# Kernel optimization log

Hardware: AMD Instinct MI355X
Metric: run time of the kernel (lower is better)

## Reference

```python
import jax, jax.numpy as jnp
import numpy as np

B, S, D, V = 2, 2048, 1024, 32000
EPSILON = 5.0


def setup_inputs() -> dict:
    key = jax.random.key(0)
    k1, k2, k3, k4 = jax.random.split(key, 4)
    inputs_embeds = jax.random.normal(k1, (B, S, D), dtype=jnp.float32)
    table = jax.random.normal(k2, (V, D), dtype=jnp.float32)
    # dx-privacy noise: unit-norm Gaussian direction * Gamma(alpha=D, rate=eps*D) scalar sample
    noise_v = jax.random.normal(k3, (B, S, D), dtype=jnp.float32)
    norm = jnp.linalg.norm(noise_v, axis=-1, keepdims=True)
    norm = jnp.where(norm > 0, norm, jnp.ones_like(norm))
    gamma_scale = jax.random.gamma(k4, jnp.float32(D)) / jnp.float32(EPSILON * D)
    noise = gamma_scale * (noise_v / norm)
    return {"inputs_embeds": inputs_embeds, "table": table, "noise": noise}


def reference(inputs_embeds, table, noise):
    # perturb embeddings with precomputed dx-privacy noise (no_grad in original)
    perturbed = inputs_embeds + noise                      # [B,S,D]
    # full similarity matrix vs vocabulary, then nearest-embedding snap
    sims = jnp.einsum('bsd,vd->bsv', perturbed, table)     # [B,S,V]
    max_token = jnp.argmax(sims, axis=-1)                  # [B,S] int
    res = jnp.take(table, max_token, axis=0)               # [B,S,D]
    return res
```

## Files before the change

kernel.cpp:

```cpp
#include <hip/hip_runtime.h>
#include <stdint.h>

#define ROWS 4096
#define DIM 1024
#define VOCAB 32000
#define BM 128
#define BN 128
#define NTILES (VOCAB / BN)
#define NCHUNKS 24
#define SCALE 2048.0f

typedef float floatx4 __attribute__((ext_vector_type(4)));
typedef _Float16 f16x8 __attribute__((ext_vector_type(8)));
typedef _Float16 f16x4 __attribute__((ext_vector_type(4)));

__device__ __forceinline__ void load_lds16(const _Float16* g, _Float16* l) {
    __builtin_amdgcn_global_load_lds(
        (const __attribute__((address_space(1))) uint32_t*)g,
        (__attribute__((address_space(3))) uint32_t*)l, 16, 0, 0);
}

__global__ void init_keys(unsigned long long* __restrict__ keys) {
    int i = blockIdx.x * 256 + threadIdx.x;
    if (i < ROWS) keys[i] = 0ull;
}

__global__ void split_sum(const float* __restrict__ x, const float* __restrict__ y,
                          _Float16* __restrict__ hi, _Float16* __restrict__ lo) {
    size_t i = ((size_t)blockIdx.x * 256 + threadIdx.x) * 8;
    floatx4 a = *(const floatx4*)(x + i);
    floatx4 b = *(const floatx4*)(x + i + 4);
    floatx4 c = *(const floatx4*)(y + i);
    floatx4 d = *(const floatx4*)(y + i + 4);
    f16x8 h, l;
#pragma unroll
    for (int j = 0; j < 4; j++) {
        float p = (a[j] + c[j]) * SCALE;
        _Float16 hh = (_Float16)p;
        h[j] = hh; l[j] = (_Float16)(p - (float)hh);
        float q = (b[j] + d[j]) * SCALE;
        _Float16 hq = (_Float16)q;
        h[4 + j] = hq; l[4 + j] = (_Float16)(q - (float)hq);
    }
    *(f16x8*)(hi + i) = h;
    *(f16x8*)(lo + i) = l;
}

__global__ void split_one(const float* __restrict__ x,
                          _Float16* __restrict__ hi, _Float16* __restrict__ lo) {
    size_t i = ((size_t)blockIdx.x * 256 + threadIdx.x) * 8;
    floatx4 a = *(const floatx4*)(x + i);
    floatx4 b = *(const floatx4*)(x + i + 4);
    f16x8 h, l;
#pragma unroll
    for (int j = 0; j < 4; j++) {
        float p = a[j] * SCALE;
        _Float16 hh = (_Float16)p;
        h[j] = hh; l[j] = (_Float16)(p - (float)hh);
        float q = b[j] * SCALE;
        _Float16 hq = (_Float16)q;
        h[4 + j] = hq; l[4 + j] = (_Float16)(q - (float)hq);
    }
    *(f16x8*)(hi + i) = h;
    *(f16x8*)(lo + i) = l;
}

__global__ __launch_bounds__(256, 3) void gemm_argmax_pre(
    const _Float16* __restrict__ Ah, const _Float16* __restrict__ Al,
    const _Float16* __restrict__ Bh, const _Float16* __restrict__ Bl,
    unsigned long long* __restrict__ keys) {
    __shared__ __align__(16) _Float16 sAh[BM * 32];
    __shared__ __align__(16) _Float16 sAl[BM * 32];
    __shared__ __align__(16) _Float16 sBh[BN * 32];
    __shared__ __align__(16) _Float16 sBl[BN * 32];
    __shared__ unsigned long long redk[BM];

    const int tid = threadIdx.x;
    const int w = tid >> 6, lane = tid & 63;
    const int quad = lane >> 4, lq = lane & 15;
    const int rb = blockIdx.x / NCHUNKS, chunk = blockIdx.x % NCHUNKS;
    const int row0 = rb * BM;
    const int wm = (w & 1) * 64, wn = (w >> 1) * 64;
    const int tstart = chunk * NTILES / NCHUNKS;
    const int tend = (chunk + 1) * NTILES / NCHUNKS;

    if (tid < BM) redk[tid] = 0ull;

    union PF { f16x8 v; _Float16 s[8]; } fidx, fone;
#pragma unroll
    for (int j = 0; j < 8; j++) { fidx.s[j] = (_Float16)0.0f; fone.s[j] = (_Float16)0.0f; }
    if (quad == 0) { fidx.s[0] = (_Float16)(float)lq; fone.s[0] = (_Float16)1.0f; }
    floatx4 c1 = {0.f, 0.f, 0.f, 0.f}, c2 = {0.f, 0.f, 0.f, 0.f};
    c1 = __builtin_amdgcn_mfma_f32_16x16x32_f16(fidx.v, fone.v, c1, 0, 0, 0);
    c2 = __builtin_amdgcn_mfma_f32_16x16x32_f16(fone.v, fidx.v, c2, 0, 0, 0);
    int m_of[4], n_of[4];
#pragma unroll
    for (int r = 0; r < 4; r++) {
        m_of[r] = (int)(c1[r] + 0.5f);
        n_of[r] = (int)(c2[r] + 0.5f);
    }

    const _Float16* gsrcA = (w == 0) ? (Ah + (size_t)row0 * DIM)
                        : (w == 1) ? (Al + (size_t)row0 * DIM)
                        : (w == 2) ? Bh : Bl;
    _Float16* ldst = (w == 0) ? sAh : (w == 1) ? sAl : (w == 2) ? sBh : sBl;

    float rmax[16];
    int ridx[16];
#pragma unroll
    for (int i = 0; i < 16; i++) { rmax[i] = -3.4e38f; ridx[i] = 0; }

    for (int t = tstart; t < tend; ++t) {
        const int n0 = t * BN;
        const _Float16* gsrc = (w < 2) ? gsrcA : (gsrcA + (size_t)n0 * DIM);
        floatx4 acc[4][4];
#pragma unroll
        for (int mi = 0; mi < 4; mi++)
#pragma unroll
            for (int ni = 0; ni < 4; ni++)
#pragma unroll
                for (int r = 0; r < 4; r++) acc[mi][ni][r] = 0.0f;

        for (int kt = 0; kt < DIM / 32; ++kt) {
            const int k0 = kt * 32;
            __syncthreads();
#pragma unroll
            for (int c = 0; c < 8; c++) {
                const _Float16* g =
                    gsrc + (size_t)(c * 16 + (lane >> 2)) * DIM + k0 + (lane & 3) * 8;
                load_lds16(g, ldst + c * 512);
            }
            __syncthreads();

            f16x8 ahf[4], alf[4];
#pragma unroll
            for (int i = 0; i < 4; i++) {
                int r = wm + i * 16 + lq;
                ahf[i] = *(const f16x8*)(sAh + r * 32 + quad * 8);
                alf[i] = *(const f16x8*)(sAl + r * 32 + quad * 8);
            }
#pragma unroll
            for (int ni = 0; ni < 4; ni++) {
                int r = wn + ni * 16 + lq;
                f16x8 bh = *(const f16x8*)(sBh + r * 32 + quad * 8);
                f16x8 bl = *(const f16x8*)(sBl + r * 32 + quad * 8);
#pragma unroll
                for (int mi = 0; mi < 4; mi++) {
                    acc[mi][ni] = __builtin_amdgcn_mfma_f32_16x16x32_f16(
                        ahf[mi], bh, acc[mi][ni], 0, 0, 0);
                    acc[mi][ni] = __builtin_amdgcn_mfma_f32_16x16x32_f16(
                        ahf[mi], bl, acc[mi][ni], 0, 0, 0);
                    acc[mi][ni] = __builtin_amdgcn_mfma_f32_16x16x32_f16(
                        alf[mi], bh, acc[mi][ni], 0, 0, 0);
                }
            }
        }
#pragma unroll
        for (int mi = 0; mi < 4; mi++)
#pragma unroll
            for (int ni = 0; ni < 4; ni++)
#pragma unroll
                for (int r = 0; r < 4; r++) {
                    float v = acc[mi][ni][r];
                    int col = n0 + wn + ni * 16 + n_of[r];
                    int s = mi * 4 + r;
                    if (v > rmax[s] || (v == rmax[s] && col < ridx[s])) {
                        rmax[s] = v;
                        ridx[s] = col;
                    }
                }
    }

#pragma unroll
    for (int s = 0; s < 16; ++s) {
        int mi = s >> 2, r = s & 3;
        int rowl = wm + mi * 16 + m_of[r];
        union { float f; uint32_t i; } u;
        u.f = rmax[s];
        uint32_t ord = (u.i & 0x80000000u) ? ~u.i : (u.i | 0x80000000u);
        unsigned long long key =
            ((unsigned long long)ord << 32) | (uint32_t)(~(uint32_t)ridx[s]);
        atomicMax(&redk[rowl], key);
    }
    __syncthreads();
    if (tid < BM) atomicMax(&keys[row0 + tid], redk[tid]);
}

#define BKF 64
#define LDKF 72
#define TILES_PER_WGF 10
#define NCHUNKSF 25

__global__ __launch_bounds__(256, 2) void gemm_argmax_fused(
    const float* __restrict__ emb, const float* __restrict__ noi,
    const float* __restrict__ table, unsigned long long* __restrict__ keys) {
    __shared__ __align__(16) _Float16 Ah[BM * LDKF];
    __shared__ __align__(16) _Float16 Al[BM * LDKF];
    __shared__ __align__(16) _Float16 Bh[BN * LDKF];
    __shared__ __align__(16) _Float16 Bl[BN * LDKF];
    __shared__ unsigned long long redk[BM];

    const int tid = threadIdx.x;
    const int wave = tid >> 6, lane = tid & 63;
    const int quad = lane >> 4, lq = lane & 15;
    const int rb = blockIdx.x / NCHUNKSF, chunk = blockIdx.x % NCHUNKSF;
    const int row0 = rb * BM;
    const int wm = (wave & 1) * 64, wn = (wave >> 1) * 64;

    if (tid < BM) redk[tid] = 0ull;

    union PF { f16x8 v; _Float16 s[8]; } fidx, fone;
#pragma unroll
    for (int j = 0; j < 8; j++) { fidx.s[j] = (_Float16)0.0f; fone.s[j] = (_Float16)0.0f; }
    if (quad == 0) { fidx.s[0] = (_Float16)(float)lq; fone.s[0] = (_Float16)1.0f; }
    floatx4 c1 = {0.f, 0.f, 0.f, 0.f}, c2 = {0.f, 0.f, 0.f, 0.f};
    c1 = __builtin_amdgcn_mfma_f32_16x16x32_f16(fidx.v, fone.v, c1, 0, 0, 0);
    c2 = __builtin_amdgcn_mfma_f32_16x16x32_f16(fone.v, fidx.v, c2, 0, 0, 0);
    int m_of[4], n_of[4];
#pragma unroll
    for (int r = 0; r < 4; r++) {
        m_of[r] = (int)(c1[r] + 0.5f);
        n_of[r] = (int)(c2[r] + 0.5f);
    }

    float rmax[16];
    int ridx[16];
#pragma unroll
    for (int i = 0; i < 16; i++) { rmax[i] = -3.4e38f; ridx[i] = 0; }

    for (int t = 0; t < TILES_PER_WGF; ++t) {
        const int n0 = (chunk * TILES_PER_WGF + t) * BN;
        floatx4 acc[4][4];
#pragma unroll
        for (int mi = 0; mi < 4; mi++)
#pragma unroll
            for (int ni = 0; ni < 4; ni++)
#pragma unroll
                for (int r = 0; r < 4; r++) acc[mi][ni][r] = 0.0f;

        for (int kt = 0; kt < DIM / BKF; ++kt) {
            const int k0 = kt * BKF;
            __syncthreads();
#pragma unroll
            for (int i = 0; i < 8; i++) {
                int c = i * 256 + tid;
                int r = c >> 4, q = c & 15;
                floatx4 e = *(const floatx4*)(emb + (size_t)(row0 + r) * DIM + k0 + q * 4);
                floatx4 n = *(const floatx4*)(noi + (size_t)(row0 + r) * DIM + k0 + q * 4);
                floatx4 b = *(const floatx4*)(table + (size_t)(n0 + r) * DIM + k0 + q * 4);
                f16x4 ah, al, bh, bl;
#pragma unroll
                for (int j = 0; j < 4; j++) {
                    float pa = (e[j] + n[j]) * SCALE;
                    _Float16 h = (_Float16)pa;
                    ah[j] = h;
                    al[j] = (_Float16)(pa - (float)h);
                    float pb = b[j] * SCALE;
                    _Float16 hb = (_Float16)pb;
                    bh[j] = hb;
                    bl[j] = (_Float16)(pb - (float)hb);
                }
                *(f16x4*)(Ah + r * LDKF + q * 4) = ah;
                *(f16x4*)(Al + r * LDKF + q * 4) = al;
                *(f16x4*)(Bh + r * LDKF + q * 4) = bh;
                *(f16x4*)(Bl + r * LDKF + q * 4) = bl;
            }
            __syncthreads();
#pragma unroll
            for (int ks = 0; ks < BKF; ks += 32) {
                f16x8 bhf[4], blf[4], ahf[4], alf[4];
#pragma unroll
                for (int i = 0; i < 4; i++) {
                    bhf[i] = *(const f16x8*)(Bh + (wn + i * 16 + lq) * LDKF + ks + quad * 8);
                    blf[i] = *(const f16x8*)(Bl + (wn + i * 16 + lq) * LDKF + ks + quad * 8);
                    ahf[i] = *(const f16x8*)(Ah + (wm + i * 16 + lq) * LDKF + ks + quad * 8);
                    alf[i] = *(const f16x8*)(Al + (wm + i * 16 + lq) * LDKF + ks + quad * 8);
                }
#pragma unroll
                for (int mi = 0; mi < 4; mi++)
#pragma unroll
                    for (int ni = 0; ni < 4; ni++) {
                        acc[mi][ni] = __builtin_amdgcn_mfma_f32_16x16x32_f16(
                            ahf[mi], bhf[ni], acc[mi][ni], 0, 0, 0);
                        acc[mi][ni] = __builtin_amdgcn_mfma_f32_16x16x32_f16(
                            ahf[mi], blf[ni], acc[mi][ni], 0, 0, 0);
                        acc[mi][ni] = __builtin_amdgcn_mfma_f32_16x16x32_f16(
                            alf[mi], bhf[ni], acc[mi][ni], 0, 0, 0);
                    }
            }
        }
#pragma unroll
        for (int mi = 0; mi < 4; mi++)
#pragma unroll
            for (int ni = 0; ni < 4; ni++)
#pragma unroll
                for (int r = 0; r < 4; r++) {
                    float v = acc[mi][ni][r];
                    int col = n0 + wn + ni * 16 + n_of[r];
                    int s = mi * 4 + r;
                    if (v > rmax[s] || (v == rmax[s] && col < ridx[s])) {
                        rmax[s] = v;
                        ridx[s] = col;
                    }
                }
    }

#pragma unroll
    for (int s = 0; s < 16; ++s) {
        int mi = s >> 2, r = s & 3;
        int rowl = wm + mi * 16 + m_of[r];
        union { float f; uint32_t i; } u;
        u.f = rmax[s];
        uint32_t ord = (u.i & 0x80000000u) ? ~u.i : (u.i | 0x80000000u);
        unsigned long long key =
            ((unsigned long long)ord << 32) | (uint32_t)(~(uint32_t)ridx[s]);
        atomicMax(&redk[rowl], key);
    }
    __syncthreads();
    if (tid < BM) atomicMax(&keys[row0 + tid], redk[tid]);
}

__global__ void gather_kernel(const unsigned long long* __restrict__ keys,
                              const float* __restrict__ table,
                              float* __restrict__ out) {
    int row = blockIdx.x;
    unsigned long long key = keys[row];
    uint32_t ix = ~(uint32_t)(key & 0xFFFFFFFFull);
    const floatx4* src = (const floatx4*)(table + (size_t)ix * DIM);
    floatx4* dst = (floatx4*)(out + (size_t)row * DIM);
    dst[threadIdx.x] = src[threadIdx.x];
}

extern "C" void kernel_launch(void* const* d_in, const int* in_sizes, int n_in,
                              void* d_out, int out_size, void* d_ws, size_t ws_size,
                              hipStream_t stream) {
    (void)in_sizes; (void)n_in; (void)out_size;
    const float* emb = (const float*)d_in[0];
    const float* table = (const float*)d_in[1];
    const float* noi = (const float*)d_in[2];
    float* out = (float*)d_out;

    uint8_t* ws = (uint8_t*)d_ws;
    unsigned long long* keys = (unsigned long long*)ws;
    const size_t keysB = (size_t)ROWS * 8;
    const size_t aB = (size_t)ROWS * DIM * 2;
    const size_t bB = (size_t)VOCAB * DIM * 2;
    const size_t need = keysB + 2 * aB + 2 * bB;

    init_keys<<<ROWS / 256, 256, 0, stream>>>(keys);

    if (ws_size >= need) {
        _Float16* Ah = (_Float16*)(ws + keysB);
        _Float16* Al = (_Float16*)(ws + keysB + aB);
        _Float16* Bh = (_Float16*)(ws + keysB + 2 * aB);
        _Float16* Bl = (_Float16*)(ws + keysB + 2 * aB + bB);
        split_sum<<<ROWS * DIM / 8 / 256, 256, 0, stream>>>(emb, noi, Ah, Al);
        split_one<<<VOCAB * DIM / 8 / 256, 256, 0, stream>>>(table, Bh, Bl);
        gemm_argmax_pre<<<(ROWS / BM) * NCHUNKS, 256, 0, stream>>>(Ah, Al, Bh, Bl, keys);
    } else {
        gemm_argmax_fused<<<(ROWS / BM) * NCHUNKSF, 256, 0, stream>>>(emb, noi, table, keys);
    }
    gather_kernel<<<ROWS, 256, 0, stream>>>(keys, table, out);
}
```

Baseline: 1.005 ms.

## Double-buffer LDS tiles in split-f16 GEMM argmax and fuse prep kernels

Double-buffers the shared-memory tiles in the GEMM-argmax kernel, so the async global-to-LDS loads for the next k-step are issued before computing the current one. Waits use explicit vmcnt/lgkmcnt counters and raw barriers in place of two __syncthreads per step. The LDS load layout changes so each 16-row group is contiguous, and MFMA sections raise wave priority. The key init and the two split kernels are merged into one prep launch, and the chunk count drops to 16 with launch bounds lowered to 2 blocks per CU to make room for the doubled LDS. This cuts launch count and load latency, at the cost of occupancy and fewer blocks in the grid.

```diff
diff --git a/kernel.cpp b/kernel.cpp
--- a/kernel.cpp
+++ b/kernel.cpp
@@ -7,7 +7,7 @@
 #define BM 128
 #define BN 128
 #define NTILES (VOCAB / BN)
-#define NCHUNKS 24
+#define NCHUNKS 16
 #define SCALE 2048.0f
 
 typedef float floatx4 __attribute__((ext_vector_type(4)));
@@ -25,54 +25,59 @@
     if (i < ROWS) keys[i] = 0ull;
 }
 
-__global__ void split_sum(const float* __restrict__ x, const float* __restrict__ y,
-                          _Float16* __restrict__ hi, _Float16* __restrict__ lo) {
-    size_t i = ((size_t)blockIdx.x * 256 + threadIdx.x) * 8;
-    floatx4 a = *(const floatx4*)(x + i);
-    floatx4 b = *(const floatx4*)(x + i + 4);
-    floatx4 c = *(const floatx4*)(y + i);
-    floatx4 d = *(const floatx4*)(y + i + 4);
-    f16x8 h, l;
-#pragma unroll
-    for (int j = 0; j < 4; j++) {
-        float p = (a[j] + c[j]) * SCALE;
-        _Float16 hh = (_Float16)p;
-        h[j] = hh; l[j] = (_Float16)(p - (float)hh);
-        float q = (b[j] + d[j]) * SCALE;
-        _Float16 hq = (_Float16)q;
-        h[4 + j] = hq; l[4 + j] = (_Float16)(q - (float)hq);
-    }
-    *(f16x8*)(hi + i) = h;
-    *(f16x8*)(lo + i) = l;
-}
-
-__global__ void split_one(const float* __restrict__ x,
-                          _Float16* __restrict__ hi, _Float16* __restrict__ lo) {
-    size_t i = ((size_t)blockIdx.x * 256 + threadIdx.x) * 8;
-    floatx4 a = *(const floatx4*)(x + i);
-    floatx4 b = *(const floatx4*)(x + i + 4);
-    f16x8 h, l;
-#pragma unroll
-    for (int j = 0; j < 4; j++) {
-        float p = a[j] * SCALE;
-        _Float16 hh = (_Float16)p;
-        h[j] = hh; l[j] = (_Float16)(p - (float)hh);
-        float q = b[j] * SCALE;
-        _Float16 hq = (_Float16)q;
-        h[4 + j] = hq; l[4 + j] = (_Float16)(q - (float)hq);
-    }
-    *(f16x8*)(hi + i) = h;
-    *(f16x8*)(lo + i) = l;
-}
-
-__global__ __launch_bounds__(256, 3) void gemm_argmax_pre(
+__global__ void prep(const float* __restrict__ emb, const float* __restrict__ noi,
+                     const float* __restrict__ table,
+                     _Float16* __restrict__ Ah, _Float16* __restrict__ Al,
+                     _Float16* __restrict__ Bh, _Float16* __restrict__ Bl,
+                     unsigned long long* __restrict__ keys) {
+    const int bid = blockIdx.x;
+    const int ABLK = ROWS * DIM / 8 / 256;
+    if (bid < ABLK) {
+        if (bid < ROWS / 256) keys[bid * 256 + threadIdx.x] = 0ull;
+        size_t i = ((size_t)bid * 256 + threadIdx.x) * 8;
+        floatx4 a = *(const floatx4*)(emb + i);
+        floatx4 b = *(const floatx4*)(emb + i + 4);
+        floatx4 c = *(const floatx4*)(noi + i);
+        floatx4 d = *(const floatx4*)(noi + i + 4);
+        f16x8 h, l;
+#pragma unroll
+        for (int j = 0; j < 4; j++) {
+            float p = (a[j] + c[j]) * SCALE;
+            _Float16 hh = (_Float16)p;
+            h[j] = hh; l[j] = (_Float16)(p - (float)hh);
+            float q = (b[j] + d[j]) * SCALE;
+            _Float16 hq = (_Float16)q;
+            h[4 + j] = hq; l[4 + j] = (_Float16)(q - (float)hq);
+        }
+        *(f16x8*)(Ah + i) = h;
+        *(f16x8*)(Al + i) = l;
+    } else {
+        size_t i = ((size_t)(bid - ABLK) * 256 + threadIdx.x) * 8;
+        floatx4 a = *(const floatx4*)(table + i);
+        floatx4 b = *(const floatx4*)(table + i + 4);
+        f16x8 h, l;
+#pragma unroll
+        for (int j = 0; j < 4; j++) {
+            float p = a[j] * SCALE;
+            _Float16 hh = (_Float16)p;
+            h[j] = hh; l[j] = (_Float16)(p - (float)hh);
+            float q = b[j] * SCALE;
+            _Float16 hq = (_Float16)q;
+            h[4 + j] = hq; l[4 + j] = (_Float16)(q - (float)hq);
+        }
+        *(f16x8*)(Bh + i) = h;
+        *(f16x8*)(Bl + i) = l;
+    }
+}
+
+__global__ __launch_bounds__(256, 2) void gemm_argmax_pre(
     const _Float16* __restrict__ Ah, const _Float16* __restrict__ Al,
     const _Float16* __restrict__ Bh, const _Float16* __restrict__ Bl,
     unsigned long long* __restrict__ keys) {
-    __shared__ __align__(16) _Float16 sAh[BM * 32];
-    __shared__ __align__(16) _Float16 sAl[BM * 32];
-    __shared__ __align__(16) _Float16 sBh[BN * 32];
-    __shared__ __align__(16) _Float16 sBl[BN * 32];
+    __shared__ __align__(16) _Float16 sAh[2][BM * 32];
+    __shared__ __align__(16) _Float16 sAl[2][BM * 32];
+    __shared__ __align__(16) _Float16 sBh[2][BN * 32];
+    __shared__ __align__(16) _Float16 sBl[2][BN * 32];
     __shared__ unsigned long long redk[BM];
 
     const int tid = threadIdx.x;
@@ -80,7 +85,8 @@
     const int quad = lane >> 4, lq = lane & 15;
     const int rb = blockIdx.x / NCHUNKS, chunk = blockIdx.x % NCHUNKS;
     const int row0 = rb * BM;
-    const int wm = (w & 1) * 64, wn = (w >> 1) * 64;
+    const int wmb = (w & 1) * 4, wnb = (w >> 1) * 4;
+    const int wm = wmb * 16, wn = wnb * 16;
     const int tstart = chunk * NTILES / NCHUNKS;
     const int tend = (chunk + 1) * NTILES / NCHUNKS;
 
@@ -100,19 +106,34 @@
         n_of[r] = (int)(c2[r] + 0.5f);
     }
 
-    const _Float16* gsrcA = (w == 0) ? (Ah + (size_t)row0 * DIM)
+    const _Float16* gbase = (w == 0) ? (Ah + (size_t)row0 * DIM)
                         : (w == 1) ? (Al + (size_t)row0 * DIM)
                         : (w == 2) ? Bh : Bl;
-    _Float16* ldst = (w == 0) ? sAh : (w == 1) ? sAl : (w == 2) ? sBh : sBl;
+    _Float16* lbase = (w == 0) ? sAh[0] : (w == 1) ? sAl[0] : (w == 2) ? sBh[0] : sBl[0];
+    const size_t g_lane = (size_t)(lane & 15) * DIM + (size_t)(lane >> 4) * 8;
+    const int loff = quad * 128 + lq * 8;
+    const bool isB = (w >= 2);
 
     float rmax[16];
     int ridx[16];
 #pragma unroll
     for (int i = 0; i < 16; i++) { rmax[i] = -3.4e38f; ridx[i] = 0; }
 
+#define STAGE(buf, t, kt)                                                        \
+    do {                                                                         \
+        const _Float16* gs_ = gbase + (isB ? (size_t)(t) * BN * DIM : 0)         \
+                              + (kt) * 32 + g_lane;                              \
+        _Float16* ld_ = lbase + (buf) * (BM * 32);                               \
+        _Pragma("unroll")                                                        \
+        for (int c_ = 0; c_ < 8; c_++)                                           \
+            load_lds16(gs_ + (size_t)(c_ * 16) * DIM, ld_ + c_ * 512);           \
+    } while (0)
+
+    int cur = 0;
+    STAGE(0, tstart, 0);
+
     for (int t = tstart; t < tend; ++t) {
         const int n0 = t * BN;
-        const _Float16* gsrc = (w < 2) ? gsrcA : (gsrcA + (size_t)n0 * DIM);
         floatx4 acc[4][4];
 #pragma unroll
         for (int mi = 0; mi < 4; mi++)
@@ -122,28 +143,27 @@
                 for (int r = 0; r < 4; r++) acc[mi][ni][r] = 0.0f;
 
         for (int kt = 0; kt < DIM / 32; ++kt) {
-            const int k0 = kt * 32;
-            __syncthreads();
-#pragma unroll
-            for (int c = 0; c < 8; c++) {
-                const _Float16* g =
-                    gsrc + (size_t)(c * 16 + (lane >> 2)) * DIM + k0 + (lane & 3) * 8;
-                load_lds16(g, ldst + c * 512);
-            }
-            __syncthreads();
-
+            int nt_ = t, nk = kt + 1;
+            if (nk == DIM / 32) { nk = 0; ++nt_; }
+            if (nt_ < tend) {
+                STAGE(cur ^ 1, nt_, nk);
+                asm volatile("s_waitcnt vmcnt(8)" ::: "memory");
+            } else {
+                asm volatile("s_waitcnt vmcnt(0)" ::: "memory");
+            }
+            __builtin_amdgcn_s_barrier();
+
+            __builtin_amdgcn_s_setprio(1);
             f16x8 ahf[4], alf[4];
 #pragma unroll
             for (int i = 0; i < 4; i++) {
-                int r = wm + i * 16 + lq;
-                ahf[i] = *(const f16x8*)(sAh + r * 32 + quad * 8);
-                alf[i] = *(const f16x8*)(sAl + r * 32 + quad * 8);
+                ahf[i] = *(const f16x8*)(&sAh[cur][(wmb + i) * 512 + loff]);
+                alf[i] = *(const f16x8*)(&sAl[cur][(wmb + i) * 512 + loff]);
             }
 #pragma unroll
             for (int ni = 0; ni < 4; ni++) {
-                int r = wn + ni * 16 + lq;
-                f16x8 bh = *(const f16x8*)(sBh + r * 32 + quad * 8);
-                f16x8 bl = *(const f16x8*)(sBl + r * 32 + quad * 8);
+                f16x8 bh = *(const f16x8*)(&sBh[cur][(wnb + ni) * 512 + loff]);
+                f16x8 bl = *(const f16x8*)(&sBl[cur][(wnb + ni) * 512 + loff]);
 #pragma unroll
                 for (int mi = 0; mi < 4; mi++) {
                     acc[mi][ni] = __builtin_amdgcn_mfma_f32_16x16x32_f16(
@@ -154,6 +174,11 @@
                         alf[mi], bh, acc[mi][ni], 0, 0, 0);
                 }
             }
+            __builtin_amdgcn_s_setprio(0);
+
+            asm volatile("s_waitcnt lgkmcnt(0)" ::: "memory");
+            __builtin_amdgcn_s_barrier();
+            cur ^= 1;
         }
 #pragma unroll
         for (int mi = 0; mi < 4; mi++)
@@ -170,6 +195,7 @@
                     }
                 }
     }
+#undef STAGE
 
 #pragma unroll
     for (int s = 0; s < 16; ++s) {
@@ -347,17 +373,17 @@
     const size_t bB = (size_t)VOCAB * DIM * 2;
     const size_t need = keysB + 2 * aB + 2 * bB;
 
-    init_keys<<<ROWS / 256, 256, 0, stream>>>(keys);
-
     if (ws_size >= need) {
         _Float16* Ah = (_Float16*)(ws + keysB);
         _Float16* Al = (_Float16*)(ws + keysB + aB);
         _Float16* Bh = (_Float16*)(ws + keysB + 2 * aB);
         _Float16* Bl = (_Float16*)(ws + keysB + 2 * aB + bB);
-        split_sum<<<ROWS * DIM / 8 / 256, 256, 0, stream>>>(emb, noi, Ah, Al);
-        split_one<<<VOCAB * DIM / 8 / 256, 256, 0, stream>>>(table, Bh, Bl);
+        const int ablk = ROWS * DIM / 8 / 256;
+        const int bblk = VOCAB * DIM / 8 / 256;
+        prep<<<ablk + bblk, 256, 0, stream>>>(emb, noi, table, Ah, Al, Bh, Bl, keys);
         gemm_argmax_pre<<<(ROWS / BM) * NCHUNKS, 256, 0, stream>>>(Ah, Al, Bh, Bl, keys);
     } else {
+        init_keys<<<ROWS / 256, 256, 0, stream>>>(keys);
         gemm_argmax_fused<<<(ROWS / BM) * NCHUNKSF, 256, 0, stream>>>(emb, noi, table, keys);
     }
     gather_kernel<<<ROWS, 256, 0, stream>>>(keys, table, out);
```

Measured after the change: 1.177 ms. +17.1%, slower.
